# Kernel optimization log

Measured on AMD Instinct MI355X. Metric: run time of the kernel, lower is better.

The kernel has to match this reference:

```python
import jax, jax.numpy as jnp
import numpy as np

B, S, D = 1, 2048, 4096
H, KV = 32, 8
HD = D // H          # 128
N_REP = H // KV      # 4
ROPE_THETA = 10000.0


def setup_inputs() -> dict:
    key = jax.random.key(0)
    ks = jax.random.split(key, 5)
    x = jax.random.normal(ks[0], (B, S, D), dtype=jnp.float32)
    wq = jax.random.normal(ks[1], (H * HD, D), dtype=jnp.float32) * 0.02
    wk = jax.random.normal(ks[2], (KV * HD, D), dtype=jnp.float32) * 0.02
    wv = jax.random.normal(ks[3], (KV * HD, D), dtype=jnp.float32) * 0.02
    wo = jax.random.normal(ks[4], (D, H * HD), dtype=jnp.float32) * 0.02
    # precomputed RoPE frequencies: freqs_cis = exp(i * t * theta_j)
    inv_freq = 1.0 / (ROPE_THETA ** (np.arange(0, HD, 2, dtype=np.float32) / HD))  # [HD/2]
    angles = np.arange(S, dtype=np.float32)[:, None] * inv_freq[None, :]           # [S, HD/2]
    freqs_cos = jnp.asarray(np.cos(angles))
    freqs_sin = jnp.asarray(np.sin(angles))
    return {"x": x, "freqs_cos": freqs_cos, "freqs_sin": freqs_sin,
            "wq": wq, "wk": wk, "wv": wv, "wo": wo}


def _rope(t, cos, sin):
    # t: [B,S,h,HD]; even/odd interleaved pairs form complex numbers
    tr, ti = t[..., 0::2], t[..., 1::2]                 # [B,S,h,HD/2]
    cos = cos[None, :, None, :]
    sin = sin[None, :, None, :]
    out = jnp.stack([tr * cos - ti * sin, tr * sin + ti * cos], axis=-1)
    return out.reshape(t.shape)


def reference(x, freqs_cos, freqs_sin, wq, wk, wv, wo):
    bs, seqlen, _ = x.shape
    xq = jnp.einsum('bsd,ed->bse', x, wq).reshape(bs, seqlen, H, HD)
    xk = jnp.einsum('bsd,ed->bse', x, wk).reshape(bs, seqlen, KV, HD)
    xv = jnp.einsum('bsd,ed->bse', x, wv).reshape(bs, seqlen, KV, HD)
    xq = _rope(xq, freqs_cos, freqs_sin)
    xk = _rope(xk, freqs_cos, freqs_sin)
    # repeat_kv: GQA expand kv heads by n_rep
    keys = jnp.repeat(xk, N_REP, axis=2)    # [B,S,H,HD]
    values = jnp.repeat(xv, N_REP, axis=2)
    scale = 1.0 / np.sqrt(HD).astype(np.float32)
    scores = jnp.einsum('bshd,bthd->bhst', xq, keys) * scale  # [B,H,S,S]
    causal = jnp.tril(jnp.ones((seqlen, seqlen), dtype=bool))
    scores = jnp.where(causal[None, None], scores, jnp.finfo(scores.dtype).min)
    attn = jax.nn.softmax(scores, axis=-1)
    out = jnp.einsum('bhst,bthd->bshd', attn, values).reshape(bs, seqlen, H * HD)
    return jnp.einsum('bse,de->bsd', out, wo)
```

## Files before the change

kernel.cpp:

```cpp
#include <hip/hip_runtime.h>
#include <hip/hip_bf16.h>
#include <stdint.h>

#define SEQ   2048
#define DM    4096
#define NH    32
#define NKV   8
#define HD    128
#define DKV   1024

typedef __attribute__((ext_vector_type(8))) short bf8_t;
typedef __attribute__((ext_vector_type(4))) float f4_t;
typedef __attribute__((ext_vector_type(16))) float f16x;

__device__ __forceinline__ short f2bf(float f) {
  union { float f; uint32_t u; } v; v.f = f;
  uint32_t r = v.u + 0x7FFFu + ((v.u >> 16) & 1u);
  return (short)(r >> 16);
}
__device__ __forceinline__ float bf2f(short s) {
  union { uint32_t u; float f; } v; v.u = ((uint32_t)(uint16_t)s) << 16;
  return v.f;
}
__device__ __forceinline__ uint32_t cvtpk(float lo, float hi) {
  uint32_t r;
  asm("v_cvt_pk_bf16_f32 %0, %1, %2" : "=v"(r) : "v"(lo), "v"(hi));
  return r;
}

__device__ __forceinline__ void async_copy16(const void* gsrc, void* ldst) {
  auto g = reinterpret_cast<const __attribute__((address_space(1))) uint32_t*>(
      reinterpret_cast<uintptr_t>(gsrc));
  auto l = reinterpret_cast<__attribute__((address_space(3))) uint32_t*>(
      reinterpret_cast<uintptr_t>(ldst));
  __builtin_amdgcn_global_load_lds(g, l, 16, 0, 0);
}

__device__ __forceinline__ f4_t mfma16(bf8_t a, bf8_t b, f4_t c) {
  return __builtin_amdgcn_mfma_f32_16x16x32_bf16(a, b, c, 0, 0, 0);
}
__device__ __forceinline__ f16x mfma32(bf8_t a, bf8_t b, f16x c) {
  return __builtin_amdgcn_mfma_f32_32x32x16_bf16(a, b, c, 0, 0, 0);
}

template<int N> __device__ __forceinline__ void vmwait();
template<> __device__ __forceinline__ void vmwait<3>() {
  asm volatile("s_waitcnt vmcnt(3)" ::: "memory");
}
template<> __device__ __forceinline__ void vmwait<4>() {
  asm volatile("s_waitcnt vmcnt(4)" ::: "memory");
}

__global__ void cvt_all_kernel(const float* __restrict__ x,
                               const float* __restrict__ wq,
                               const float* __restrict__ wk,
                               const float* __restrict__ wv,
                               const float* __restrict__ wo,
                               short* __restrict__ out)
{
  const int E0 = SEQ * DM / 4;
  const int E1 = E0 + DM * DM / 4;
  const int E2 = E1 + DKV * DM / 4;
  const int E3 = E2 + DKV * DM / 4;
  const int E4 = E3 + DM * DM / 4;
  const int stride = gridDim.x * blockDim.x;
  for (int i = blockIdx.x * blockDim.x + threadIdx.x; i < E4; i += stride) {
    const float4* src; int off;
    if (i < E0)      { src = (const float4*)x;  off = i; }
    else if (i < E1) { src = (const float4*)wq; off = i - E0; }
    else if (i < E2) { src = (const float4*)wk; off = i - E1; }
    else if (i < E3) { src = (const float4*)wv; off = i - E2; }
    else             { src = (const float4*)wo; off = i - E3; }
    float4 v = src[off];
    short4 o;
    o.x = f2bf(v.x); o.y = f2bf(v.y); o.z = f2bf(v.z); o.w = f2bf(v.w);
    ((short4*)out)[i] = o;
  }
}

template<int MODE, int BM, int BN>
__global__ __launch_bounds__(512, 2)
void gemm8_kernel(const short* __restrict__ A,
                  const short* __restrict__ Bw,
                  float* __restrict__ Cf,
                  short* __restrict__ Cq,
                  short* __restrict__ Ck,
                  short* __restrict__ Cv)
{
  constexpr int MREP = BM / 32;
  constexpr int SPP  = MREP / 4;
  constexpr int AJ   = BM / 128;
  constexpr int SB   = BN / 64;
  constexpr int NT   = DM / 64;

  __shared__ short As[2][BM * 64];
  __shared__ short Bs[2][BN * 64];

  const int tid = threadIdx.x, lane = tid & 63, wid = tid >> 6;
  const int wr = wid >> 2, wn = wid & 3;
  const int cl = lane & 15, kh = lane >> 4;
  const int row0 = blockIdx.y * BM;
  const int col0 = blockIdx.x * BN;

  f4_t acc[MREP][SB];
  #pragma unroll
  for (int i = 0; i < MREP; i++)
    #pragma unroll
    for (int j = 0; j < SB; j++) { acc[i][j][0]=0.f; acc[i][j][1]=0.f; acc[i][j][2]=0.f; acc[i][j][3]=0.f; }

  auto STGA = [&](short* T, int h, int kt) {
    #pragma unroll
    for (int j = 0; j < AJ; ++j) {
      const int c = wid * (64 * AJ) + j * 64 + lane;
      const int row = h * (BM / 2) + (c >> 3), pcol = c & 7;
      const int lcol = pcol ^ (row & 7);
      async_copy16(&A[(size_t)(row0 + row) * DM + kt * 64 + lcol * 8],
                   &T[(h * (BM * 4) + c) * 8]);
    }
  };
  auto STGB = [&](short* T, int sl, int kt) {
    const int c = wid * 64 + lane;
    const int row = sl * 64 + (c >> 3), pcol = c & 7;
    const int lcol = pcol ^ (row & 7);
    async_copy16(&Bw[(size_t)(col0 + row) * DM + kt * 64 + lcol * 8],
                 &T[(sl * 512 + c) * 8]);
  };

  bf8_t bF[SB][2];
  bf8_t aF[SPP][2];
  auto LDA = [&](const short* T, int ms0) {
    #pragma unroll
    for (int s = 0; s < SPP; ++s)
      #pragma unroll
      for (int q = 0; q < 2; ++q) {
        const int row = wr * (BM / 2) + (ms0 + s) * 16 + cl;
        const int pcol = (q * 4 + kh) ^ (row & 7);
        aF[s][q] = *(const bf8_t*)&T[(row * 8 + pcol) * 8];
      }
  };
  auto LDB = [&](const short* T) {
    #pragma unroll
    for (int n = 0; n < SB; ++n)
      #pragma unroll
      for (int q = 0; q < 2; ++q) {
        const int row = wn * (16 * SB) + n * 16 + cl;
        const int pcol = (q * 4 + kh) ^ (row & 7);
        bF[n][q] = *(const bf8_t*)&T[(row * 8 + pcol) * 8];
      }
  };

#define PHASE(TA, TB, PH, READB, STGSTMT, VMC)                                \
  {                                                                           \
    LDA(TA, (PH) * SPP);                                                      \
    if (READB) LDB(TB);                                                       \
    STGSTMT                                                                   \
    __builtin_amdgcn_s_barrier();                                             \
    asm volatile("s_waitcnt lgkmcnt(0)" ::: "memory");                        \
    __builtin_amdgcn_s_setprio(1);                                            \
    _Pragma("unroll")                                                         \
    for (int s_ = 0; s_ < SPP; ++s_) {                                        \
      _Pragma("unroll")                                                       \
      for (int n_ = 0; n_ < SB; ++n_) {                                       \
        _Pragma("unroll")                                                     \
        for (int q_ = 0; q_ < 2; ++q_)                                        \
          acc[(PH) * SPP + s_][n_] =                                          \
              mfma16(aF[s_][q_], bF[n_][q_], acc[(PH) * SPP + s_][n_]);       \
      }                                                                       \
    }                                                                         \
    __builtin_amdgcn_s_setprio(0);                                            \
    if (VMC) vmwait<SB>();                                                    \
    __builtin_amdgcn_s_barrier();                                             \
  }

  #pragma unroll
  for (int sl = 0; sl < SB; ++sl) STGB(Bs[0], sl, 0);
  STGA(As[0], 0, 0); STGA(As[0], 1, 0);
  #pragma unroll
  for (int sl = 0; sl < SB; ++sl) STGB(Bs[1], sl, 1);
  vmwait<SB>();
  __builtin_amdgcn_s_barrier();

  for (int i = 0; i < NT / 2; ++i) {
    const int tA1 = 2 * i + 1;
    int t2 = 2 * i + 2; if (t2 > NT - 1) t2 = NT - 1;
    int t3 = 2 * i + 3; if (t3 > NT - 1) t3 = NT - 1;
    if constexpr (SB == 4) {
      PHASE(As[0], Bs[0], 0, true,  { STGA(As[1], 0, tA1); STGA(As[1], 1, tA1); }, false);
      PHASE(As[0], Bs[0], 1, false, { STGB(Bs[0], 0, t2); STGB(Bs[0], 1, t2); }, false);
      PHASE(As[0], Bs[0], 2, false, { STGB(Bs[0], 2, t2); STGB(Bs[0], 3, t2); }, false);
      PHASE(As[0], Bs[0], 3, false, { }, true);
      PHASE(As[1], Bs[1], 0, true,  { STGA(As[0], 0, t2); STGA(As[0], 1, t2); }, false);
      PHASE(As[1], Bs[1], 1, false, { STGB(Bs[1], 0, t3); STGB(Bs[1], 1, t3); }, false);
      PHASE(As[1], Bs[1], 2, false, { STGB(Bs[1], 2, t3); STGB(Bs[1], 3, t3); }, false);
      PHASE(As[1], Bs[1], 3, false, { }, true);
    } else {
      PHASE(As[0], Bs[0], 0, true,  { STGA(As[1], 0, tA1); STGA(As[1], 1, tA1); }, false);
      PHASE(As[0], Bs[0], 1, false, { STGB(Bs[0], 0, t2); }, false);
      PHASE(As[0], Bs[0], 2, false, { STGB(Bs[0], 1, t2); }, false);
      PHASE(As[0], Bs[0], 3, false, { STGB(Bs[0], 2, t2); }, true);
      PHASE(As[1], Bs[1], 0, true,  { STGA(As[0], 0, t2); STGA(As[0], 1, t2); }, false);
      PHASE(As[1], Bs[1], 1, false, { STGB(Bs[1], 0, t3); }, false);
      PHASE(As[1], Bs[1], 2, false, { STGB(Bs[1], 1, t3); }, false);
      PHASE(As[1], Bs[1], 3, false, { STGB(Bs[1], 2, t3); }, true);
    }
  }
#undef PHASE

  const int rb = kh * 4;
  #pragma unroll
  for (int mi = 0; mi < MREP; mi++) {
    const int m0 = row0 + wr * (BM / 2) + mi * 16 + rb;
    #pragma unroll
    for (int ni = 0; ni < SB; ni++) {
      const int n = col0 + wn * (16 * SB) + ni * 16 + cl;
      if (MODE == 0) {
        #pragma unroll
        for (int r = 0; r < 4; r++) Cf[(size_t)(m0 + r) * DM + n] = acc[mi][ni][r];
      } else if (n < DM) {
        #pragma unroll
        for (int r = 0; r < 4; r++) Cq[(size_t)(m0 + r) * DM + n] = f2bf(acc[mi][ni][r]);
      } else if (n < DM + DKV) {
        const int nk = n - DM;
        #pragma unroll
        for (int r = 0; r < 4; r++) Ck[(size_t)(m0 + r) * DKV + nk] = f2bf(acc[mi][ni][r]);
      } else {
        const int nv = n - DM - DKV;
        short4 pk;
        pk.x = f2bf(acc[mi][ni][0]); pk.y = f2bf(acc[mi][ni][1]);
        pk.z = f2bf(acc[mi][ni][2]); pk.w = f2bf(acc[mi][ni][3]);
        *(short4*)&Cv[(size_t)nv * SEQ + m0] = pk;
      }
    }
  }
}

__global__ void rope_kernel(short* __restrict__ Qb, short* __restrict__ Kb,
                            const float* __restrict__ fcos, const float* __restrict__ fsin)
{
  const int NQP = SEQ * (DM / 2);
  const int NKP = SEQ * (DKV / 2);
  int idx = blockIdx.x * blockDim.x + threadIdx.x;
  if (idx >= NQP + NKP) return;
  short* T; int s, p, rowlen;
  if (idx < NQP) { T = Qb; s = idx >> 11; p = idx & 2047; rowlen = DM; }
  else { int j = idx - NQP; T = Kb; s = j >> 9; p = j & 511; rowlen = DKV; }
  const int h = p >> 6, i = p & 63;
  const float c  = fcos[s * 64 + i];
  const float sn = fsin[s * 64 + i];
  const size_t base = (size_t)s * rowlen + h * HD + 2 * i;
  const float e = bf2f(T[base]), o = bf2f(T[base + 1]);
  T[base]     = f2bf(e * c - o * sn);
  T[base + 1] = f2bf(e * sn + o * c);
}

__device__ __forceinline__ void flash_stage(const short* __restrict__ Kb,
                                            const short* __restrict__ Vt,
                                            short* Kl, short* Vl,
                                            int kv0, int hkv, int wid, int lane)
{
  #pragma unroll
  for (int i = 0; i < 4; ++i) {
    int c = wid * 256 + i * 64 + lane;
    int row = c >> 4, pos = c & 15;
    int dc = pos ^ (row & 7);
    async_copy16(&Kb[(size_t)(kv0 + row) * DKV + hkv * HD + dc * 8], &Kl[c * 8]);
  }
  #pragma unroll
  for (int i = 0; i < 4; ++i) {
    int c = wid * 256 + i * 64 + lane;
    int row = c >> 3, pos = c & 7;
    int kc = pos ^ (row & 7);
    async_copy16(&Vt[(size_t)(hkv * HD + row) * SEQ + kv0 + kc * 8], &Vl[c * 8]);
  }
}

union U4B8 { uint32_t w[4]; bf8_t v; };

__device__ __forceinline__ void flash_compute(const short* __restrict__ Kl,
                                              const short* __restrict__ Vl,
                                              const bf8_t* qF, f16x* accO,
                                              float& m_run, float& l_run,
                                              int kv0, int qw0, int c31, int hi)
{
  const float scale = 0.08838834764831845f;

  f16x accS[2];
  #pragma unroll
  for (int nu = 0; nu < 2; ++nu) {
    #pragma unroll
    for (int r = 0; r < 16; ++r) accS[nu][r] = 0.f;
  }
  #pragma unroll
  for (int nu = 0; nu < 2; ++nu) {
    const int row = nu * 32 + c31, rx = row & 7;
    #pragma unroll
    for (int s = 0; s < 8; ++s) {
      const int pos = (2 * s + hi) ^ rx;
      bf8_t kf = *(const bf8_t*)&Kl[row * 128 + pos * 8];
      accS[nu] = mfma32(kf, qF[s], accS[nu]);
    }
  }

  if (kv0 + 63 > qw0) {
    const int q_abs = qw0 + c31;
    #pragma unroll
    for (int nu = 0; nu < 2; ++nu)
      #pragma unroll
      for (int r = 0; r < 16; ++r) {
        const int kv_abs = kv0 + 32 * nu + (r & 3) + 8 * (r >> 2) + 4 * hi;
        if (kv_abs > q_abs) accS[nu][r] = -3.0e38f;
      }
  }

  float rm = -3.0e38f;
  #pragma unroll
  for (int nu = 0; nu < 2; ++nu)
    #pragma unroll
    for (int r = 0; r < 16; ++r) rm = fmaxf(rm, accS[nu][r]);
  rm = fmaxf(rm, __shfl_xor(rm, 32));
  const float pmax = rm * scale;
  if (!__all(pmax - m_run <= 8.0f)) {
    const float mnew = fmaxf(m_run, pmax);
    const float corr = __expf(m_run - mnew);
    m_run = mnew;
    l_run *= corr;
    #pragma unroll
    for (int dt = 0; dt < 4; ++dt)
      #pragma unroll
      for (int r = 0; r < 16; ++r) accO[dt][r] *= corr;
  }

  float tsum = 0.f;
  uint32_t u[8][2];
  #pragma unroll
  for (int m = 0; m < 8; ++m) {
    const int nu = m >> 2, rb = 4 * (m & 3);
    float p0 = __expf(fmaf(accS[nu][rb + 0], scale, -m_run));
    float p1 = __expf(fmaf(accS[nu][rb + 1], scale, -m_run));
    float p2 = __expf(fmaf(accS[nu][rb + 2], scale, -m_run));
    float p3 = __expf(fmaf(accS[nu][rb + 3], scale, -m_run));
    tsum += (p0 + p1) + (p2 + p3);
    u[m][0] = cvtpk(p0, p1);
    u[m][1] = cvtpk(p2, p3);
  }
  l_run += tsum + __shfl_xor(tsum, 32);

  bf8_t pa[4];
  #pragma unroll
  for (int ks = 0; ks < 4; ++ks) {
    const uint32_t a0 = u[2 * ks][0],     a1 = u[2 * ks][1];
    const uint32_t b0 = u[2 * ks + 1][0], b1 = u[2 * ks + 1][1];
    const uint32_t mp0 = hi ? a0 : b0, mp1 = hi ? a1 : b1;
    const uint32_t s0 = __shfl_xor(mp0, 32), s1 = __shfl_xor(mp1, 32);
    U4B8 f;
    f.w[0] = hi ? s0 : a0;
    f.w[1] = hi ? s1 : a1;
    f.w[2] = hi ? b0 : s0;
    f.w[3] = hi ? b1 : s1;
    pa[ks] = f.v;
  }

  #pragma unroll
  for (int dt = 0; dt < 4; ++dt) {
    const int row = dt * 32 + c31, rx = row & 7;
    #pragma unroll
    for (int ks = 0; ks < 4; ++ks) {
      const int pos = (2 * ks + hi) ^ rx;
      bf8_t vf = *(const bf8_t*)&Vl[row * 64 + pos * 8];
      accO[dt] = mfma32(vf, pa[ks], accO[dt]);
    }
  }
}

__global__ __launch_bounds__(256, 2)
void flash_kernel(const short* __restrict__ Qb,
                  const short* __restrict__ Kb,
                  const short* __restrict__ Vt,
                  short* __restrict__ Ob)
{
  __shared__ short Kl0[64 * 128], Kl1[64 * 128];
  __shared__ short Vl0[128 * 64], Vl1[128 * 64];

  const int tid = threadIdx.x, lane = tid & 63, wid = tid >> 6;
  const int c31 = lane & 31, hi = lane >> 5;

  const int b = blockIdx.x;
  const int pairid = b & 255, halfsel = b >> 8;
  const int h = pairid >> 3, p = pairid & 7;
  const int qt = halfsel ? (15 - p) : p;
  const int q0 = qt * 128;
  const int hkv = h >> 2;
  const int qw0 = q0 + wid * 32;

  bf8_t qF[8];
  {
    const size_t qb = (size_t)(qw0 + c31) * DM + h * HD + hi * 8;
    #pragma unroll
    for (int s = 0; s < 8; ++s) qF[s] = *(const bf8_t*)&Qb[qb + s * 16];
  }

  f16x accO[4];
  #pragma unroll
  for (int dt = 0; dt < 4; ++dt)
    #pragma unroll
    for (int r = 0; r < 16; ++r) accO[dt][r] = 0.f;
  float m_run = -INFINITY, l_run = 0.f;

  const int nt = (q0 >> 6) + 2;

  flash_stage(Kb, Vt, Kl0, Vl0, 0, hkv, wid, lane);
  __syncthreads();
  for (int t = 0; t < nt; t += 2) {
    flash_stage(Kb, Vt, Kl1, Vl1, (t + 1) * 64, hkv, wid, lane);
    if (t * 64 <= qw0 + 31)
      flash_compute(Kl0, Vl0, qF, accO, m_run, l_run, t * 64, qw0, c31, hi);
    __syncthreads();
    if (t + 2 < nt) flash_stage(Kb, Vt, Kl0, Vl0, (t + 2) * 64, hkv, wid, lane);
    if ((t + 1) * 64 <= qw0 + 31)
      flash_compute(Kl1, Vl1, qF, accO, m_run, l_run, (t + 1) * 64, qw0, c31, hi);
    __syncthreads();
  }

  short* Ol = (wid < 2) ? &Kl0[wid * 4096] : &Kl1[(wid - 2) * 4096];
  const float oinv = 1.0f / l_run;
  #pragma unroll
  for (int dt = 0; dt < 4; ++dt)
    #pragma unroll
    for (int w = 0; w < 8; ++w) {
      const int r = 2 * w;
      const int d0 = (r & 3) + 8 * (r >> 2) + 4 * hi + dt * 32;
      const uint32_t pk = cvtpk(accO[dt][r] * oinv, accO[dt][r + 1] * oinv);
      const int pos = (d0 >> 3) ^ (c31 & 7);
      *(uint32_t*)&Ol[c31 * 128 + pos * 8 + (d0 & 7)] = pk;
    }
  __syncthreads();
  const int rowq = lane >> 1;
  #pragma unroll
  for (int i = 0; i < 8; ++i) {
    const int dc = (lane & 1) * 8 + i;
    const int pos = dc ^ (rowq & 7);
    int4 v = *(const int4*)&Ol[rowq * 128 + pos * 8];
    *(int4*)&Ob[(size_t)(q0 + wid * 32 + rowq) * DM + h * HD + dc * 8] = v;
  }
}

extern "C" void kernel_launch(void* const* d_in, const int* in_sizes, int n_in,
                              void* d_out, int out_size, void* d_ws, size_t ws_size,
                              hipStream_t stream)
{
  const float* x    = (const float*)d_in[0];
  const float* fcos = (const float*)d_in[1];
  const float* fsin = (const float*)d_in[2];
  const float* wq   = (const float*)d_in[3];
  const float* wk   = (const float*)d_in[4];
  const float* wv   = (const float*)d_in[5];
  const float* wo   = (const float*)d_in[6];
  float* out = (float*)d_out;

  char* p = (char*)d_ws;
  short* xb  = (short*)p; p += (size_t)SEQ * DM * 2;
  short* wqb = (short*)p; p += (size_t)DM * DM * 2;
  short* wkb = (short*)p; p += (size_t)DKV * DM * 2;
  short* wvb = (short*)p; p += (size_t)DKV * DM * 2;
  short* wob = (short*)p; p += (size_t)DM * DM * 2;
  short* Qb  = (short*)p; p += (size_t)SEQ * DM * 2;
  short* Kb  = (short*)p; p += (size_t)SEQ * DKV * 2;
  short* Vt  = (short*)p; p += (size_t)DKV * SEQ * 2;
  short* Ab  = (short*)p; p += (size_t)SEQ * DM * 2;
  (void)wkb; (void)wvb;

  cvt_all_kernel<<<2048, 256, 0, stream>>>(x, wq, wk, wv, wo, xb);

  gemm8_kernel<1, 256, 192><<<dim3(32, 8), 512, 0, stream>>>(xb, wqb,
                                                             nullptr, Qb, Kb, Vt);
  rope_kernel<<<20480, 256, 0, stream>>>(Qb, Kb, fcos, fsin);
  flash_kernel<<<512, 256, 0, stream>>>(Qb, Kb, Vt, Ab);
  gemm8_kernel<0, 128, 256><<<dim3(16, 16), 512, 0, stream>>>(Ab, wob,
                                                              out, nullptr, nullptr, nullptr);
}
```

Baseline: 278.1 us.

## Fuse RoPE into QKV GEMM epilogue, retune output GEMM pipeline, add MFMA priority

Applies the rotary embedding inside the QKV projection epilogue, using a lane shuffle to fetch the paired even/odd element, and drops the separate rope kernel along with its read-modify-write pass over Q and K. The output-projection GEMM (SB==4) now runs two phases per buffer instead of four, with more rows per phase and all B staging issued in one phase. The flash attention MFMA loops are wrapped in s_setprio so matrix instructions get issue priority. Risks include extra cos/sin loads in the epilogue and a coarser pipeline that may overlap loads less well.

```diff
diff --git a/kernel.cpp b/kernel.cpp
--- a/kernel.cpp
+++ b/kernel.cpp
@@ -82,15 +82,17 @@
 __global__ __launch_bounds__(512, 2)
 void gemm8_kernel(const short* __restrict__ A,
                   const short* __restrict__ Bw,
+                  const float* __restrict__ fcos,
+                  const float* __restrict__ fsin,
                   float* __restrict__ Cf,
                   short* __restrict__ Cq,
                   short* __restrict__ Ck,
                   short* __restrict__ Cv)
 {
   constexpr int MREP = BM / 32;
-  constexpr int SPP  = MREP / 4;
+  constexpr int SB   = BN / 64;
+  constexpr int SPP  = (SB == 4) ? 2 : (MREP / 4);
   constexpr int AJ   = BM / 128;
-  constexpr int SB   = BN / 64;
   constexpr int NT   = DM / 64;
 
   __shared__ short As[2][BM * 64];
@@ -186,13 +188,11 @@
     int t3 = 2 * i + 3; if (t3 > NT - 1) t3 = NT - 1;
     if constexpr (SB == 4) {
       PHASE(As[0], Bs[0], 0, true,  { STGA(As[1], 0, tA1); STGA(As[1], 1, tA1); }, false);
-      PHASE(As[0], Bs[0], 1, false, { STGB(Bs[0], 0, t2); STGB(Bs[0], 1, t2); }, false);
-      PHASE(As[0], Bs[0], 2, false, { STGB(Bs[0], 2, t2); STGB(Bs[0], 3, t2); }, false);
-      PHASE(As[0], Bs[0], 3, false, { }, true);
+      PHASE(As[0], Bs[0], 1, false, { STGB(Bs[0], 0, t2); STGB(Bs[0], 1, t2);
+                                      STGB(Bs[0], 2, t2); STGB(Bs[0], 3, t2); }, true);
       PHASE(As[1], Bs[1], 0, true,  { STGA(As[0], 0, t2); STGA(As[0], 1, t2); }, false);
-      PHASE(As[1], Bs[1], 1, false, { STGB(Bs[1], 0, t3); STGB(Bs[1], 1, t3); }, false);
-      PHASE(As[1], Bs[1], 2, false, { STGB(Bs[1], 2, t3); STGB(Bs[1], 3, t3); }, false);
-      PHASE(As[1], Bs[1], 3, false, { }, true);
+      PHASE(As[1], Bs[1], 1, false, { STGB(Bs[1], 0, t3); STGB(Bs[1], 1, t3);
+                                      STGB(Bs[1], 2, t3); STGB(Bs[1], 3, t3); }, true);
     } else {
       PHASE(As[0], Bs[0], 0, true,  { STGA(As[1], 0, tA1); STGA(As[1], 1, tA1); }, false);
       PHASE(As[0], Bs[0], 1, false, { STGB(Bs[0], 0, t2); }, false);
@@ -216,13 +216,19 @@
       if (MODE == 0) {
         #pragma unroll
         for (int r = 0; r < 4; r++) Cf[(size_t)(m0 + r) * DM + n] = acc[mi][ni][r];
-      } else if (n < DM) {
+      } else if (n < DM + DKV) {
+        const int fi = (n & 127) >> 1;
+        const float sgn = (n & 1) ? 1.0f : -1.0f;
         #pragma unroll
-        for (int r = 0; r < 4; r++) Cq[(size_t)(m0 + r) * DM + n] = f2bf(acc[mi][ni][r]);
-      } else if (n < DM + DKV) {
-        const int nk = n - DM;
-        #pragma unroll
-        for (int r = 0; r < 4; r++) Ck[(size_t)(m0 + r) * DKV + nk] = f2bf(acc[mi][ni][r]);
+        for (int r = 0; r < 4; r++) {
+          const float own = acc[mi][ni][r];
+          const float par = __shfl_xor(own, 1);
+          const float cv = fcos[(m0 + r) * 64 + fi];
+          const float sv = fsin[(m0 + r) * 64 + fi];
+          const float v = fmaf(sgn * par, sv, own * cv);
+          if (n < DM) Cq[(size_t)(m0 + r) * DM + n] = f2bf(v);
+          else        Ck[(size_t)(m0 + r) * DKV + (n - DM)] = f2bf(v);
+        }
       } else {
         const int nv = n - DM - DKV;
         short4 pk;
@@ -234,25 +240,6 @@
   }
 }
 
-__global__ void rope_kernel(short* __restrict__ Qb, short* __restrict__ Kb,
-                            const float* __restrict__ fcos, const float* __restrict__ fsin)
-{
-  const int NQP = SEQ * (DM / 2);
-  const int NKP = SEQ * (DKV / 2);
-  int idx = blockIdx.x * blockDim.x + threadIdx.x;
-  if (idx >= NQP + NKP) return;
-  short* T; int s, p, rowlen;
-  if (idx < NQP) { T = Qb; s = idx >> 11; p = idx & 2047; rowlen = DM; }
-  else { int j = idx - NQP; T = Kb; s = j >> 9; p = j & 511; rowlen = DKV; }
-  const int h = p >> 6, i = p & 63;
-  const float c  = fcos[s * 64 + i];
-  const float sn = fsin[s * 64 + i];
-  const size_t base = (size_t)s * rowlen + h * HD + 2 * i;
-  const float e = bf2f(T[base]), o = bf2f(T[base + 1]);
-  T[base]     = f2bf(e * c - o * sn);
-  T[base + 1] = f2bf(e * sn + o * c);
-}
-
 __device__ __forceinline__ void flash_stage(const short* __restrict__ Kb,
                                             const short* __restrict__ Vt,
                                             short* Kl, short* Vl,
@@ -290,6 +277,7 @@
     #pragma unroll
     for (int r = 0; r < 16; ++r) accS[nu][r] = 0.f;
   }
+  __builtin_amdgcn_s_setprio(1);
   #pragma unroll
   for (int nu = 0; nu < 2; ++nu) {
     const int row = nu * 32 + c31, rx = row & 7;
@@ -300,6 +288,7 @@
       accS[nu] = mfma32(kf, qF[s], accS[nu]);
     }
   }
+  __builtin_amdgcn_s_setprio(0);
 
   if (kv0 + 63 > qw0) {
     const int q_abs = qw0 + c31;
@@ -360,6 +349,7 @@
     pa[ks] = f.v;
   }
 
+  __builtin_amdgcn_s_setprio(1);
   #pragma unroll
   for (int dt = 0; dt < 4; ++dt) {
     const int row = dt * 32 + c31, rx = row & 7;
@@ -370,6 +360,7 @@
       accO[dt] = mfma32(vf, pa[ks], accO[dt]);
     }
   }
+  __builtin_amdgcn_s_setprio(0);
 }
 
 __global__ __launch_bounds__(256, 2)
@@ -471,10 +462,9 @@
 
   cvt_all_kernel<<<2048, 256, 0, stream>>>(x, wq, wk, wv, wo, xb);
 
-  gemm8_kernel<1, 256, 192><<<dim3(32, 8), 512, 0, stream>>>(xb, wqb,
+  gemm8_kernel<1, 256, 192><<<dim3(32, 8), 512, 0, stream>>>(xb, wqb, fcos, fsin,
                                                              nullptr, Qb, Kb, Vt);
-  rope_kernel<<<20480, 256, 0, stream>>>(Qb, Kb, fcos, fsin);
   flash_kernel<<<512, 256, 0, stream>>>(Qb, Kb, Vt, Ab);
-  gemm8_kernel<0, 128, 256><<<dim3(16, 16), 512, 0, stream>>>(Ab, wob,
+  gemm8_kernel<0, 128, 256><<<dim3(16, 16), 512, 0, stream>>>(Ab, wob, fcos, fsin,
                                                               out, nullptr, nullptr, nullptr);
 }
```

Result: slower. 292.4 us (+5.2%).

## Fuse fp32-to-bf16 weight conversion into GEMM B-tile loads via registers

Applied to the files above, without the earlier changes.

Drops the separate pass that converts the weights to bf16. The GEMMs now load fp32 weights straight from global memory into registers, convert them to bf16 and write them to LDS, with the global loads issued two phases ahead in a register double buffer. This removes a full write-then-read round trip of about 40M weight elements to workspace. In exchange each GEMM block reads twice the weight bytes, pays for conversion ALU work and register pressure, and gives up the async global-to-LDS copies for B.

```diff
diff --git a/kernel.cpp b/kernel.cpp
--- a/kernel.cpp
+++ b/kernel.cpp
@@ -44,34 +44,19 @@
 }
 
 template<int N> __device__ __forceinline__ void vmwait();
-template<> __device__ __forceinline__ void vmwait<3>() {
-  asm volatile("s_waitcnt vmcnt(3)" ::: "memory");
-}
-template<> __device__ __forceinline__ void vmwait<4>() {
-  asm volatile("s_waitcnt vmcnt(4)" ::: "memory");
-}
-
-__global__ void cvt_all_kernel(const float* __restrict__ x,
-                               const float* __restrict__ wq,
-                               const float* __restrict__ wk,
-                               const float* __restrict__ wv,
-                               const float* __restrict__ wo,
-                               short* __restrict__ out)
-{
-  const int E0 = SEQ * DM / 4;
-  const int E1 = E0 + DM * DM / 4;
-  const int E2 = E1 + DKV * DM / 4;
-  const int E3 = E2 + DKV * DM / 4;
-  const int E4 = E3 + DM * DM / 4;
+template<> __device__ __forceinline__ void vmwait<6>() {
+  asm volatile("s_waitcnt vmcnt(6)" ::: "memory");
+}
+template<> __device__ __forceinline__ void vmwait<8>() {
+  asm volatile("s_waitcnt vmcnt(8)" ::: "memory");
+}
+
+union U4B8 { uint32_t w[4]; bf8_t v; };
+
+__global__ void cvt_x_kernel(const float* __restrict__ x, short* __restrict__ out, int n4) {
   const int stride = gridDim.x * blockDim.x;
-  for (int i = blockIdx.x * blockDim.x + threadIdx.x; i < E4; i += stride) {
-    const float4* src; int off;
-    if (i < E0)      { src = (const float4*)x;  off = i; }
-    else if (i < E1) { src = (const float4*)wq; off = i - E0; }
-    else if (i < E2) { src = (const float4*)wk; off = i - E1; }
-    else if (i < E3) { src = (const float4*)wv; off = i - E2; }
-    else             { src = (const float4*)wo; off = i - E3; }
-    float4 v = src[off];
+  for (int i = blockIdx.x * blockDim.x + threadIdx.x; i < n4; i += stride) {
+    float4 v = ((const float4*)x)[i];
     short4 o;
     o.x = f2bf(v.x); o.y = f2bf(v.y); o.z = f2bf(v.z); o.w = f2bf(v.w);
     ((short4*)out)[i] = o;
@@ -81,17 +66,20 @@
 template<int MODE, int BM, int BN>
 __global__ __launch_bounds__(512, 2)
 void gemm8_kernel(const short* __restrict__ A,
-                  const short* __restrict__ Bw,
+                  const float* __restrict__ Bw0,
+                  const float* __restrict__ Bw1,
+                  const float* __restrict__ Bw2,
                   float* __restrict__ Cf,
                   short* __restrict__ Cq,
                   short* __restrict__ Ck,
                   short* __restrict__ Cv)
 {
   constexpr int MREP = BM / 32;
+  constexpr int SB   = BN / 64;
   constexpr int SPP  = MREP / 4;
   constexpr int AJ   = BM / 128;
-  constexpr int SB   = BN / 64;
   constexpr int NT   = DM / 64;
+  constexpr int NB   = 2 * SB;
 
   __shared__ short As[2][BM * 64];
   __shared__ short Bs[2][BN * 64];
@@ -118,12 +106,36 @@
                    &T[(h * (BM * 4) + c) * 8]);
     }
   };
-  auto STGB = [&](short* T, int sl, int kt) {
+
+  float4 rA[SB][2], rB[SB][2];
+  auto LDGB = [&](float4 (*r)[2], int kt) {
+    #pragma unroll
+    for (int sl = 0; sl < SB; ++sl) {
+      const int c = wid * 64 + lane;
+      const int row = sl * 64 + (c >> 3), pcol = c & 7;
+      const int lcol = pcol ^ (row & 7);
+      const float* src;
+      if (MODE == 0) {
+        src = Bw0 + (size_t)(col0 + row) * DM;
+      } else {
+        const int rr = col0 + row;
+        src = (rr < DM)       ? (Bw0 + (size_t)rr * DM)
+            : (rr < DM + DKV) ? (Bw1 + (size_t)(rr - DM) * DM)
+                              : (Bw2 + (size_t)(rr - DM - DKV) * DM);
+      }
+      const float* g = src + kt * 64 + lcol * 8;
+      r[sl][0] = *(const float4*)g;
+      r[sl][1] = *(const float4*)(g + 4);
+    }
+  };
+  auto WRB = [&](short* T, const float4 (*r)[2], int sl) {
     const int c = wid * 64 + lane;
-    const int row = sl * 64 + (c >> 3), pcol = c & 7;
-    const int lcol = pcol ^ (row & 7);
-    async_copy16(&Bw[(size_t)(col0 + row) * DM + kt * 64 + lcol * 8],
-                 &T[(sl * 512 + c) * 8]);
+    U4B8 f;
+    f.w[0] = cvtpk(r[sl][0].x, r[sl][0].y);
+    f.w[1] = cvtpk(r[sl][0].z, r[sl][0].w);
+    f.w[2] = cvtpk(r[sl][1].x, r[sl][1].y);
+    f.w[3] = cvtpk(r[sl][1].z, r[sl][1].w);
+    *(bf8_t*)&T[(sl * 512 + c) * 8] = f.v;
   };
 
   bf8_t bF[SB][2];
@@ -168,41 +180,38 @@
       }                                                                       \
     }                                                                         \
     __builtin_amdgcn_s_setprio(0);                                            \
-    if (VMC) vmwait<SB>();                                                    \
+    if (VMC) vmwait<NB>();                                                    \
     __builtin_amdgcn_s_barrier();                                             \
   }
 
-  #pragma unroll
-  for (int sl = 0; sl < SB; ++sl) STGB(Bs[0], sl, 0);
+  LDGB(rA, 0);
+  WRB(Bs[0], rA, 0); WRB(Bs[0], rA, 1);
+  if constexpr (SB >= 3) WRB(Bs[0], rA, 2);
+  if constexpr (SB >= 4) WRB(Bs[0], rA, 3);
   STGA(As[0], 0, 0); STGA(As[0], 1, 0);
-  #pragma unroll
-  for (int sl = 0; sl < SB; ++sl) STGB(Bs[1], sl, 1);
-  vmwait<SB>();
+  LDGB(rB, 1);
+  asm volatile("s_waitcnt lgkmcnt(0)" ::: "memory");
+  vmwait<NB>();
   __builtin_amdgcn_s_barrier();
 
   for (int i = 0; i < NT / 2; ++i) {
-    const int tA1 = 2 * i + 1;
+    const int t1 = 2 * i + 1;
     int t2 = 2 * i + 2; if (t2 > NT - 1) t2 = NT - 1;
     int t3 = 2 * i + 3; if (t3 > NT - 1) t3 = NT - 1;
-    if constexpr (SB == 4) {
-      PHASE(As[0], Bs[0], 0, true,  { STGA(As[1], 0, tA1); STGA(As[1], 1, tA1); }, false);
-      PHASE(As[0], Bs[0], 1, false, { STGB(Bs[0], 0, t2); STGB(Bs[0], 1, t2); }, false);
-      PHASE(As[0], Bs[0], 2, false, { STGB(Bs[0], 2, t2); STGB(Bs[0], 3, t2); }, false);
-      PHASE(As[0], Bs[0], 3, false, { }, true);
-      PHASE(As[1], Bs[1], 0, true,  { STGA(As[0], 0, t2); STGA(As[0], 1, t2); }, false);
-      PHASE(As[1], Bs[1], 1, false, { STGB(Bs[1], 0, t3); STGB(Bs[1], 1, t3); }, false);
-      PHASE(As[1], Bs[1], 2, false, { STGB(Bs[1], 2, t3); STGB(Bs[1], 3, t3); }, false);
-      PHASE(As[1], Bs[1], 3, false, { }, true);
-    } else {
-      PHASE(As[0], Bs[0], 0, true,  { STGA(As[1], 0, tA1); STGA(As[1], 1, tA1); }, false);
-      PHASE(As[0], Bs[0], 1, false, { STGB(Bs[0], 0, t2); }, false);
-      PHASE(As[0], Bs[0], 2, false, { STGB(Bs[0], 1, t2); }, false);
-      PHASE(As[0], Bs[0], 3, false, { STGB(Bs[0], 2, t2); }, true);
-      PHASE(As[1], Bs[1], 0, true,  { STGA(As[0], 0, t2); STGA(As[0], 1, t2); }, false);
-      PHASE(As[1], Bs[1], 1, false, { STGB(Bs[1], 0, t3); }, false);
-      PHASE(As[1], Bs[1], 2, false, { STGB(Bs[1], 1, t3); }, false);
-      PHASE(As[1], Bs[1], 3, false, { STGB(Bs[1], 2, t3); }, true);
-    }
+    PHASE(As[0], Bs[0], 0, true,
+          { STGA(As[1], 0, t1); STGA(As[1], 1, t1); LDGB(rA, t2); }, false);
+    PHASE(As[0], Bs[0], 1, false, { WRB(Bs[1], rB, 0); WRB(Bs[1], rB, 1); }, false);
+    PHASE(As[0], Bs[0], 2, false,
+          { if constexpr (SB >= 3) WRB(Bs[1], rB, 2);
+            if constexpr (SB >= 4) WRB(Bs[1], rB, 3); }, false);
+    PHASE(As[0], Bs[0], 3, false, { }, true);
+    PHASE(As[1], Bs[1], 0, true,
+          { STGA(As[0], 0, t2); STGA(As[0], 1, t2); LDGB(rB, t3); }, false);
+    PHASE(As[1], Bs[1], 1, false, { WRB(Bs[0], rA, 0); WRB(Bs[0], rA, 1); }, false);
+    PHASE(As[1], Bs[1], 2, false,
+          { if constexpr (SB >= 3) WRB(Bs[0], rA, 2);
+            if constexpr (SB >= 4) WRB(Bs[0], rA, 3); }, false);
+    PHASE(As[1], Bs[1], 3, false, { }, true);
   }
 #undef PHASE
 
@@ -274,8 +283,6 @@
   }
 }
 
-union U4B8 { uint32_t w[4]; bf8_t v; };
-
 __device__ __forceinline__ void flash_compute(const short* __restrict__ Kl,
                                               const short* __restrict__ Vl,
                                               const bf8_t* qF, f16x* accO,
@@ -459,22 +466,17 @@
 
   char* p = (char*)d_ws;
   short* xb  = (short*)p; p += (size_t)SEQ * DM * 2;
-  short* wqb = (short*)p; p += (size_t)DM * DM * 2;
-  short* wkb = (short*)p; p += (size_t)DKV * DM * 2;
-  short* wvb = (short*)p; p += (size_t)DKV * DM * 2;
-  short* wob = (short*)p; p += (size_t)DM * DM * 2;
   short* Qb  = (short*)p; p += (size_t)SEQ * DM * 2;
   short* Kb  = (short*)p; p += (size_t)SEQ * DKV * 2;
   short* Vt  = (short*)p; p += (size_t)DKV * SEQ * 2;
   short* Ab  = (short*)p; p += (size_t)SEQ * DM * 2;
-  (void)wkb; (void)wvb;
-
-  cvt_all_kernel<<<2048, 256, 0, stream>>>(x, wq, wk, wv, wo, xb);
-
-  gemm8_kernel<1, 256, 192><<<dim3(32, 8), 512, 0, stream>>>(xb, wqb,
+
+  cvt_x_kernel<<<1024, 256, 0, stream>>>(x, xb, SEQ * DM / 4);
+
+  gemm8_kernel<1, 256, 192><<<dim3(32, 8), 512, 0, stream>>>(xb, wq, wk, wv,
                                                              nullptr, Qb, Kb, Vt);
   rope_kernel<<<20480, 256, 0, stream>>>(Qb, Kb, fcos, fsin);
   flash_kernel<<<512, 256, 0, stream>>>(Qb, Kb, Vt, Ab);
-  gemm8_kernel<0, 128, 256><<<dim3(16, 16), 512, 0, stream>>>(Ab, wob,
+  gemm8_kernel<0, 128, 256><<<dim3(16, 16), 512, 0, stream>>>(Ab, wo, nullptr, nullptr,
                                                               out, nullptr, nullptr, nullptr);
 }
```

Measured after the change: 343.6 us. +23.6%, slower.
